# Kernel optimization log

Hardware: AMD Instinct MI355X
Metric: run time of the kernel (lower is better)

## Reference

```python
import jax, jax.numpy as jnp
import numpy as np

CUTOFF = 32.0  # matches init_kwargs cutoff


def _reduce_single(elem, cutoff):
    """elem: [T, D]. Returns (means_padded [T, D], n_segs scalar int32).

    Faithful to the torch loop: representative = elem[0]; walk frames; when
    ||rep - frame|| > cutoff, close the segment [rep_id:f_ind] (mean over it)
    and restart at `frame`. Final open segment is also emitted. Because the
    number of segments is data-dependent, we return a fixed-shape [T, D]
    buffer whose first n_segs rows are the stacked segment means (rest zeros).
    """
    T, D = elem.shape

    def step(rep, frame):
        d = jnp.linalg.norm(rep - frame)  # torch.norm default = Frobenius/L2
        new_seg = d > cutoff
        rep = jnp.where(new_seg, frame, rep)
        return rep, new_seg

    # flags[i] == True means frame i+1 starts a new segment
    _, flags = jax.lax.scan(step, elem[0], elem[1:])
    flags = jnp.concatenate([jnp.zeros((1,), dtype=bool), flags])  # frame 0 never starts anew
    seg_id = jnp.cumsum(flags.astype(jnp.int32))  # [T], ordered segment ids
    n_segs = seg_id[-1] + 1

    sums = jax.ops.segment_sum(elem, seg_id, num_segments=T)  # [T, D]
    counts = jax.ops.segment_sum(jnp.ones((T,), elem.dtype), seg_id, num_segments=T)  # [T]
    means = sums / jnp.maximum(counts, 1.0)[:, None]  # padded rows stay 0
    return means, n_segs


def setup_inputs() -> dict:
    key = jax.random.key(0)
    batch = jax.random.normal(key, (16, 4096, 512), dtype=jnp.float32)
    return {"batch": batch}


def reference(batch):
    # vmap over the list-of-sequences batch dim (all sequences same length T)
    means, n_segs = jax.vmap(lambda e: _reduce_single(e, CUTOFF))(batch)
    return means, n_segs
```

## Files before the change

kernel.cpp:

```cpp
#include <hip/hip_runtime.h>

#define NB 16
#define NT 4096
#define ND 512
#define NLEV 12
#define UPSTRIDE 4104

#define DIST8_F32(sout, y0, y1)                                   \
    {                                                             \
        float d_;                                                 \
        d_ = r0.x - (y0).x; sout = d_ * d_;                       \
        d_ = r0.y - (y0).y; sout = fmaf(d_, d_, sout);            \
        d_ = r0.z - (y0).z; sout = fmaf(d_, d_, sout);            \
        d_ = r0.w - (y0).w; sout = fmaf(d_, d_, sout);            \
        d_ = r1.x - (y1).x; sout = fmaf(d_, d_, sout);            \
        d_ = r1.y - (y1).y; sout = fmaf(d_, d_, sout);            \
        d_ = r1.z - (y1).z; sout = fmaf(d_, d_, sout);            \
        d_ = r1.w - (y1).w; sout = fmaf(d_, d_, sout);            \
    }

__device__ __forceinline__ bool decide_exact(const float* __restrict__ base, int row,
                                             int lane, float4 r0, float4 r1) {
    const float4* fp = (const float4*)(base + (size_t)row * ND);
    float4 y0 = fp[lane];
    float4 y1 = fp[lane + 64];
    float d;
    double sd;
    d = r0.x - y0.x; sd  = (double)d * d;
    d = r0.y - y0.y; sd += (double)d * d;
    d = r0.z - y0.z; sd += (double)d * d;
    d = r0.w - y0.w; sd += (double)d * d;
    d = r1.x - y1.x; sd += (double)d * d;
    d = r1.y - y1.y; sd += (double)d * d;
    d = r1.z - y1.z; sd += (double)d * d;
    d = r1.w - y1.w; sd += (double)d * d;
    #pragma unroll
    for (int off = 32; off >= 1; off >>= 1) sd += __shfl_xor(sd, off, 64);
    return ((float)sd > 1024.0f);
}

__device__ __forceinline__ bool screen1(float sk, const float* __restrict__ base,
                                        int row, int lane, float4 r0, float4 r1) {
    if (sk > 1024.25f) return true;
    if (sk < 1023.75f) return false;
    return decide_exact(base, row, lane, r0, r1);
}

__global__ __launch_bounds__(256) void kA_next(const float* __restrict__ in,
                                               int* __restrict__ nxt) {
    int lin  = blockIdx.x * 4 + (threadIdx.x >> 6);
    int lane = threadIdx.x & 63;
    int b = lin >> 12;
    int j = lin & (NT - 1);
    const float* base = in + (size_t)b * NT * ND;
    const float4* repp = (const float4*)(base + (size_t)j * ND);
    float4 r0 = repp[lane];
    float4 r1 = repp[lane + 64];

    int result = NT;
    int i = j + 1;
    while (i < NT) {
        int row0 = i;
        int row1 = (i + 1 < NT) ? i + 1 : NT - 1;
        int row2 = (i + 2 < NT) ? i + 2 : NT - 1;
        int row3 = (i + 3 < NT) ? i + 3 : NT - 1;
        const float4* f0 = (const float4*)(base + (size_t)row0 * ND);
        const float4* f1 = (const float4*)(base + (size_t)row1 * ND);
        const float4* f2 = (const float4*)(base + (size_t)row2 * ND);
        const float4* f3 = (const float4*)(base + (size_t)row3 * ND);
        float4 a0 = f0[lane], b0 = f0[lane + 64];
        float4 a1 = f1[lane], b1 = f1[lane + 64];
        float4 a2 = f2[lane], b2 = f2[lane + 64];
        float4 a3 = f3[lane], b3 = f3[lane + 64];

        float s0, s1, s2, s3;
        DIST8_F32(s0, a0, b0);
        DIST8_F32(s1, a1, b1);
        DIST8_F32(s2, a2, b2);
        DIST8_F32(s3, a3, b3);

        #pragma unroll
        for (int off = 32; off >= 1; off >>= 1) {
            s0 += __shfl_xor(s0, off, 64);
            s1 += __shfl_xor(s1, off, 64);
            s2 += __shfl_xor(s2, off, 64);
            s3 += __shfl_xor(s3, off, 64);
        }

        int nv = NT - i;
        int found = -1;
        if (screen1(s0, base, row0, lane, r0, r1)) found = i;
        else if (nv > 1 && screen1(s1, base, row1, lane, r0, r1)) found = i + 1;
        else if (nv > 2 && screen1(s2, base, row2, lane, r0, r1)) found = i + 2;
        else if (nv > 3 && screen1(s3, base, row3, lane, r0, r1)) found = i + 3;
        if (found >= 0) { result = found; break; }
        i += 4;
    }
    if (lane == 0) nxt[b * NT + j] = result;
}

__global__ __launch_bounds__(1024) void kB_build(const int* __restrict__ nxt,
                                                 unsigned short* __restrict__ up) {
    __shared__ unsigned short cur[NT + 8];
    __shared__ unsigned short nx[NT + 8];
    int b = blockIdx.x;
    int t = threadIdx.x;
    for (int j = t; j <= NT; j += 1024)
        cur[j] = (j < NT) ? (unsigned short)nxt[b * NT + j] : (unsigned short)NT;
    __syncthreads();
    {
        unsigned short* d0 = up + (size_t)(0 * NB + b) * UPSTRIDE;
        for (int j = t; j <= NT; j += 1024) d0[j] = cur[j];
    }
    for (int k = 1; k < NLEV; ++k) {
        for (int j = t; j <= NT; j += 1024) nx[j] = cur[cur[j]];
        __syncthreads();
        for (int j = t; j <= NT; j += 1024) cur[j] = nx[j];
        __syncthreads();
        unsigned short* dk = up + (size_t)(k * NB + b) * UPSTRIDE;
        for (int j = t; j <= NT; j += 1024) dk[j] = cur[j];
    }
}

__global__ __launch_bounds__(256) void kC_descend(const unsigned short* __restrict__ up,
                                                  int* __restrict__ start,
                                                  int* __restrict__ nseg,
                                                  float* __restrict__ out_tail) {
    int idx = blockIdx.x * 256 + threadIdx.x;
    int b = idx >> 12;
    int i = idx & (NT - 1);
    int pos = 0, cnt = 0;
    #pragma unroll
    for (int k = NLEV - 1; k >= 0; --k) {
        int t = up[(size_t)(k * NB + b) * UPSTRIDE + pos];
        if (t <= i) { pos = t; cnt += (1 << k); }
    }
    if (pos == i) start[b * NT + cnt] = i;
    if (i == NT - 1) {
        nseg[b] = cnt + 1;
        out_tail[b] = (float)(cnt + 1);
    }
}

__global__ __launch_bounds__(256) void kD_means(const float* __restrict__ in,
                                                const int* __restrict__ nxt,
                                                const int* __restrict__ start,
                                                const int* __restrict__ nseg,
                                                float* __restrict__ out) {
    int wid  = threadIdx.x >> 6;
    int lane = threadIdx.x & 63;
    int g = blockIdx.x * 4 + wid;
    int L0 = g * 8;
    for (int L = L0; L < L0 + 8; ++L) {
        int b = L >> 12;
        int r = L & (NT - 1);
        float4 acc0 = make_float4(0.f, 0.f, 0.f, 0.f);
        float4 acc1 = make_float4(0.f, 0.f, 0.f, 0.f);
        int n = nseg[b];
        if (r < n) {
            int s = start[b * NT + r];
            int e = nxt[b * NT + s];
            const float4* base = (const float4*)(in + (size_t)(b * NT + s) * ND);
            int cnt = e - s;
            for (int f = 0; f < cnt; ++f) {
                float4 v0 = base[(size_t)f * (ND / 4) + lane];
                float4 v1 = base[(size_t)f * (ND / 4) + lane + 64];
                acc0.x += v0.x; acc0.y += v0.y; acc0.z += v0.z; acc0.w += v0.w;
                acc1.x += v1.x; acc1.y += v1.y; acc1.z += v1.z; acc1.w += v1.w;
            }
            float c = (float)cnt;
            acc0.x /= c; acc0.y /= c; acc0.z /= c; acc0.w /= c;
            acc1.x /= c; acc1.y /= c; acc1.z /= c; acc1.w /= c;
        }
        float4* orow = (float4*)(out + (size_t)(b * NT + r) * ND);
        orow[lane]      = acc0;
        orow[lane + 64] = acc1;
    }
}

extern "C" void kernel_launch(void* const* d_in, const int* in_sizes, int n_in,
                              void* d_out, int out_size, void* d_ws, size_t ws_size,
                              hipStream_t stream) {
    const float* in = (const float*)d_in[0];
    float* out = (float*)d_out;
    char* ws = (char*)d_ws;

    int*            nxt   = (int*)(ws + 0);
    int*            start = (int*)(ws + 262144);
    int*            nseg  = (int*)(ws + 524288);
    unsigned short* up    = (unsigned short*)(ws + 524352);

    kA_next   <<<NB * NT / 4,   256,  0, stream>>>(in, nxt);
    kB_build  <<<NB,            1024, 0, stream>>>(nxt, up);
    kC_descend<<<NB * NT / 256, 256,  0, stream>>>(up, start, nseg,
                                                   out + (size_t)NB * NT * ND);
    kD_means  <<<2048,          256,  0, stream>>>(in, nxt, start, nseg, out);
}
```

Measured before the change: 334.7 us.

## Screen first four successors per frame in one pass, defer rare long scans

The next-break search now gives each wave 16 representatives, with 4 lanes per representative each checking one candidate successor. Only ambiguous or unresolved cases go onto an atomic worklist, and a second tail kernel resumes the full scan for those. The binary-lifting table plus descend kernels are replaced by one per-batch kernel that marks reachable segment starts in a bitmap and compacts them with a prefix scan. The means kernel now runs one wave per output row and unrolls its accumulation loop by two. The cost is an extra memset and worklist atomics, and per-lane 512-float serial loads in the screening pass are uncoalesced.

```diff
diff --git a/kernel.cpp b/kernel.cpp
--- a/kernel.cpp
+++ b/kernel.cpp
@@ -4,20 +4,6 @@
 #define NT 4096
 #define ND 512
 #define NLEV 12
-#define UPSTRIDE 4104
-
-#define DIST8_F32(sout, y0, y1)                                   \
-    {                                                             \
-        float d_;                                                 \
-        d_ = r0.x - (y0).x; sout = d_ * d_;                       \
-        d_ = r0.y - (y0).y; sout = fmaf(d_, d_, sout);            \
-        d_ = r0.z - (y0).z; sout = fmaf(d_, d_, sout);            \
-        d_ = r0.w - (y0).w; sout = fmaf(d_, d_, sout);            \
-        d_ = r1.x - (y1).x; sout = fmaf(d_, d_, sout);            \
-        d_ = r1.y - (y1).y; sout = fmaf(d_, d_, sout);            \
-        d_ = r1.z - (y1).z; sout = fmaf(d_, d_, sout);            \
-        d_ = r1.w - (y1).w; sout = fmaf(d_, d_, sout);            \
-    }
 
 __device__ __forceinline__ bool decide_exact(const float* __restrict__ base, int row,
                                              int lane, float4 r0, float4 r1) {
@@ -39,6 +25,19 @@
     return ((float)sd > 1024.0f);
 }
 
+#define DIST8_F32(sout, y0, y1)                                   \
+    {                                                             \
+        float d_;                                                 \
+        d_ = r0.x - (y0).x; sout = d_ * d_;                       \
+        d_ = r0.y - (y0).y; sout = fmaf(d_, d_, sout);            \
+        d_ = r0.z - (y0).z; sout = fmaf(d_, d_, sout);            \
+        d_ = r0.w - (y0).w; sout = fmaf(d_, d_, sout);            \
+        d_ = r1.x - (y1).x; sout = fmaf(d_, d_, sout);            \
+        d_ = r1.y - (y1).y; sout = fmaf(d_, d_, sout);            \
+        d_ = r1.z - (y1).z; sout = fmaf(d_, d_, sout);            \
+        d_ = r1.w - (y1).w; sout = fmaf(d_, d_, sout);            \
+    }
+
 __device__ __forceinline__ bool screen1(float sk, const float* __restrict__ base,
                                         int row, int lane, float4 r0, float4 r1) {
     if (sk > 1024.25f) return true;
@@ -47,99 +46,164 @@
 }
 
 __global__ __launch_bounds__(256) void kA_next(const float* __restrict__ in,
-                                               int* __restrict__ nxt) {
-    int lin  = blockIdx.x * 4 + (threadIdx.x >> 6);
+                                               int* __restrict__ nxt,
+                                               int2* __restrict__ list,
+                                               int* __restrict__ cnt) {
+    int wave = blockIdx.x * 4 + (threadIdx.x >> 6);
     int lane = threadIdx.x & 63;
-    int b = lin >> 12;
-    int j = lin & (NT - 1);
+    int j0 = wave * 16;
+    int b  = j0 >> 12;
+    int js = lane >> 2;
+    int p  = lane & 3;
+    int j  = (j0 & (NT - 1)) + js;
+    int ri = j + 1 + p;
+    bool valid = ri < NT;
+    int rc = valid ? ri : j;
+
     const float* base = in + (size_t)b * NT * ND;
-    const float4* repp = (const float4*)(base + (size_t)j * ND);
-    float4 r0 = repp[lane];
-    float4 r1 = repp[lane + 64];
-
-    int result = NT;
-    int i = j + 1;
-    while (i < NT) {
-        int row0 = i;
-        int row1 = (i + 1 < NT) ? i + 1 : NT - 1;
-        int row2 = (i + 2 < NT) ? i + 2 : NT - 1;
-        int row3 = (i + 3 < NT) ? i + 3 : NT - 1;
-        const float4* f0 = (const float4*)(base + (size_t)row0 * ND);
-        const float4* f1 = (const float4*)(base + (size_t)row1 * ND);
-        const float4* f2 = (const float4*)(base + (size_t)row2 * ND);
-        const float4* f3 = (const float4*)(base + (size_t)row3 * ND);
-        float4 a0 = f0[lane], b0 = f0[lane + 64];
-        float4 a1 = f1[lane], b1 = f1[lane + 64];
-        float4 a2 = f2[lane], b2 = f2[lane + 64];
-        float4 a3 = f3[lane], b3 = f3[lane + 64];
-
-        float s0, s1, s2, s3;
-        DIST8_F32(s0, a0, b0);
-        DIST8_F32(s1, a1, b1);
-        DIST8_F32(s2, a2, b2);
-        DIST8_F32(s3, a3, b3);
-
-        #pragma unroll
-        for (int off = 32; off >= 1; off >>= 1) {
-            s0 += __shfl_xor(s0, off, 64);
-            s1 += __shfl_xor(s1, off, 64);
-            s2 += __shfl_xor(s2, off, 64);
-            s3 += __shfl_xor(s3, off, 64);
-        }
-
-        int nv = NT - i;
-        int found = -1;
-        if (screen1(s0, base, row0, lane, r0, r1)) found = i;
-        else if (nv > 1 && screen1(s1, base, row1, lane, r0, r1)) found = i + 1;
-        else if (nv > 2 && screen1(s2, base, row2, lane, r0, r1)) found = i + 2;
-        else if (nv > 3 && screen1(s3, base, row3, lane, r0, r1)) found = i + 3;
-        if (found >= 0) { result = found; break; }
-        i += 4;
-    }
-    if (lane == 0) nxt[b * NT + j] = result;
-}
-
-__global__ __launch_bounds__(1024) void kB_build(const int* __restrict__ nxt,
-                                                 unsigned short* __restrict__ up) {
-    __shared__ unsigned short cur[NT + 8];
-    __shared__ unsigned short nx[NT + 8];
+    const float4* rp = (const float4*)(base + (size_t)j  * ND);
+    const float4* xp = (const float4*)(base + (size_t)rc * ND);
+
+    float s = 0.f;
+    #pragma unroll 8
+    for (int c = 0; c < 128; ++c) {
+        float4 a = rp[c];
+        float4 x = xp[c];
+        float d;
+        d = a.x - x.x; s = fmaf(d, d, s);
+        d = a.y - x.y; s = fmaf(d, d, s);
+        d = a.z - x.z; s = fmaf(d, d, s);
+        d = a.w - x.w; s = fmaf(d, d, s);
+    }
+
+    unsigned long long yes = __ballot(valid && (s > 1024.25f));
+    unsigned long long amb = __ballot(valid && (s > 1023.75f) && (s <= 1024.25f));
+
+    if (p == 0) {
+        int bj = b * NT + j;
+        unsigned ny = (unsigned)(yes >> (js * 4)) & 0xFu;
+        unsigned na = (unsigned)(amb >> (js * 4)) & 0xFu;
+        int ry = ny ? (__ffs(ny) - 1) : 4;
+        int ra = na ? (__ffs(na) - 1) : 4;
+        if (ra < ry) {
+            int idx = atomicAdd(cnt, 1);
+            list[idx] = make_int2(bj, j + 1 + ra);
+        } else if (ry < 4) {
+            nxt[bj] = j + 1 + ry;
+        } else if (j <= NT - 6) {
+            int idx = atomicAdd(cnt, 1);
+            list[idx] = make_int2(bj, j + 5);
+        } else {
+            nxt[bj] = NT;
+        }
+    }
+}
+
+__global__ __launch_bounds__(256) void kA2_tail(const float* __restrict__ in,
+                                                const int2* __restrict__ list,
+                                                const int* __restrict__ cnt,
+                                                int* __restrict__ nxt) {
+    int wave = blockIdx.x * 4 + (threadIdx.x >> 6);
+    int lane = threadIdx.x & 63;
+    int n = *cnt;
+    for (int e = wave; e < n; e += 2048) {
+        int2 ent = list[e];
+        int bj = ent.x;
+        int b = bj >> 12, j = bj & (NT - 1);
+        const float* base = in + (size_t)b * NT * ND;
+        const float4* repp = (const float4*)(base + (size_t)j * ND);
+        float4 r0 = repp[lane];
+        float4 r1 = repp[lane + 64];
+        int result = NT;
+        int i = ent.y;
+        while (i < NT) {
+            int row0 = i;
+            int row1 = (i + 1 < NT) ? i + 1 : NT - 1;
+            int row2 = (i + 2 < NT) ? i + 2 : NT - 1;
+            int row3 = (i + 3 < NT) ? i + 3 : NT - 1;
+            const float4* f0 = (const float4*)(base + (size_t)row0 * ND);
+            const float4* f1 = (const float4*)(base + (size_t)row1 * ND);
+            const float4* f2 = (const float4*)(base + (size_t)row2 * ND);
+            const float4* f3 = (const float4*)(base + (size_t)row3 * ND);
+            float4 a0 = f0[lane], b0 = f0[lane + 64];
+            float4 a1 = f1[lane], b1 = f1[lane + 64];
+            float4 a2 = f2[lane], b2 = f2[lane + 64];
+            float4 a3 = f3[lane], b3 = f3[lane + 64];
+            float s0, s1, s2, s3;
+            DIST8_F32(s0, a0, b0);
+            DIST8_F32(s1, a1, b1);
+            DIST8_F32(s2, a2, b2);
+            DIST8_F32(s3, a3, b3);
+            #pragma unroll
+            for (int off = 32; off >= 1; off >>= 1) {
+                s0 += __shfl_xor(s0, off, 64);
+                s1 += __shfl_xor(s1, off, 64);
+                s2 += __shfl_xor(s2, off, 64);
+                s3 += __shfl_xor(s3, off, 64);
+            }
+            int nv = NT - i;
+            int found = -1;
+            if (screen1(s0, base, row0, lane, r0, r1)) found = i;
+            else if (nv > 1 && screen1(s1, base, row1, lane, r0, r1)) found = i + 1;
+            else if (nv > 2 && screen1(s2, base, row2, lane, r0, r1)) found = i + 2;
+            else if (nv > 3 && screen1(s3, base, row3, lane, r0, r1)) found = i + 3;
+            if (found >= 0) { result = found; break; }
+            i += 4;
+        }
+        if (lane == 0) nxt[bj] = result;
+    }
+}
+
+__global__ __launch_bounds__(1024) void kChain(const int* __restrict__ nxt,
+                                               int* __restrict__ start,
+                                               int* __restrict__ nseg,
+                                               float* __restrict__ out_tail) {
+    __shared__ unsigned short h[NT + 1];
+    __shared__ unsigned short h2[NT + 1];
+    __shared__ unsigned reach[NT / 32];
+    __shared__ unsigned pref[NT / 32];
+    __shared__ unsigned wsum[NT / 32];
     int b = blockIdx.x;
     int t = threadIdx.x;
     for (int j = t; j <= NT; j += 1024)
-        cur[j] = (j < NT) ? (unsigned short)nxt[b * NT + j] : (unsigned short)NT;
+        h[j] = (j < NT) ? (unsigned short)nxt[b * NT + j] : (unsigned short)NT;
+    for (int w = t; w < NT / 32; w += 1024) reach[w] = 0;
     __syncthreads();
-    {
-        unsigned short* d0 = up + (size_t)(0 * NB + b) * UPSTRIDE;
-        for (int j = t; j <= NT; j += 1024) d0[j] = cur[j];
-    }
-    for (int k = 1; k < NLEV; ++k) {
-        for (int j = t; j <= NT; j += 1024) nx[j] = cur[cur[j]];
-        __syncthreads();
-        for (int j = t; j <= NT; j += 1024) cur[j] = nx[j];
-        __syncthreads();
-        unsigned short* dk = up + (size_t)(k * NB + b) * UPSTRIDE;
-        for (int j = t; j <= NT; j += 1024) dk[j] = cur[j];
-    }
-}
-
-__global__ __launch_bounds__(256) void kC_descend(const unsigned short* __restrict__ up,
-                                                  int* __restrict__ start,
-                                                  int* __restrict__ nseg,
-                                                  float* __restrict__ out_tail) {
-    int idx = blockIdx.x * 256 + threadIdx.x;
-    int b = idx >> 12;
-    int i = idx & (NT - 1);
-    int pos = 0, cnt = 0;
-    #pragma unroll
-    for (int k = NLEV - 1; k >= 0; --k) {
-        int t = up[(size_t)(k * NB + b) * UPSTRIDE + pos];
-        if (t <= i) { pos = t; cnt += (1 << k); }
-    }
-    if (pos == i) start[b * NT + cnt] = i;
-    if (i == NT - 1) {
-        nseg[b] = cnt + 1;
-        out_tail[b] = (float)(cnt + 1);
-    }
+    if (t == 0) reach[0] = 1u;
+    __syncthreads();
+    for (int k = 0; k < NLEV; ++k) {
+        if (t < NT / 32) {
+            unsigned m = reach[t];
+            while (m) {
+                int bit = __ffs(m) - 1; m &= m - 1;
+                int d = h[t * 32 + bit];
+                if (d < NT) atomicOr(&reach[d >> 5], 1u << (d & 31));
+            }
+        }
+        __syncthreads();
+        for (int j = t; j <= NT; j += 1024) h2[j] = h[h[j]];
+        __syncthreads();
+        for (int j = t; j <= NT; j += 1024) h[j] = h2[j];
+        __syncthreads();
+    }
+    if (t < NT / 32) { wsum[t] = __popc(reach[t]); pref[t] = wsum[t]; }
+    __syncthreads();
+    for (int off = 1; off < NT / 32; off <<= 1) {
+        unsigned v = 0;
+        if (t < NT / 32 && t >= off) v = pref[t - off];
+        __syncthreads();
+        if (t < NT / 32) pref[t] += v;
+        __syncthreads();
+    }
+    int n = pref[NT / 32 - 1];
+    for (int j = t; j < NT; j += 1024) {
+        unsigned w = reach[j >> 5];
+        if (w & (1u << (j & 31))) {
+            int r = (int)(pref[j >> 5] - __popc(w) + __popc(w & ((1u << (j & 31)) - 1)));
+            start[b * NT + r] = j;
+        }
+    }
+    if (t == 0) { nseg[b] = n; out_tail[b] = (float)n; }
 }
 
 __global__ __launch_bounds__(256) void kD_means(const float* __restrict__ in,
@@ -147,35 +211,42 @@
                                                 const int* __restrict__ start,
                                                 const int* __restrict__ nseg,
                                                 float* __restrict__ out) {
-    int wid  = threadIdx.x >> 6;
+    int wave = blockIdx.x * 4 + (threadIdx.x >> 6);
     int lane = threadIdx.x & 63;
-    int g = blockIdx.x * 4 + wid;
-    int L0 = g * 8;
-    for (int L = L0; L < L0 + 8; ++L) {
-        int b = L >> 12;
-        int r = L & (NT - 1);
-        float4 acc0 = make_float4(0.f, 0.f, 0.f, 0.f);
-        float4 acc1 = make_float4(0.f, 0.f, 0.f, 0.f);
-        int n = nseg[b];
-        if (r < n) {
-            int s = start[b * NT + r];
-            int e = nxt[b * NT + s];
-            const float4* base = (const float4*)(in + (size_t)(b * NT + s) * ND);
-            int cnt = e - s;
-            for (int f = 0; f < cnt; ++f) {
-                float4 v0 = base[(size_t)f * (ND / 4) + lane];
-                float4 v1 = base[(size_t)f * (ND / 4) + lane + 64];
-                acc0.x += v0.x; acc0.y += v0.y; acc0.z += v0.z; acc0.w += v0.w;
-                acc1.x += v1.x; acc1.y += v1.y; acc1.z += v1.z; acc1.w += v1.w;
-            }
-            float c = (float)cnt;
-            acc0.x /= c; acc0.y /= c; acc0.z /= c; acc0.w /= c;
-            acc1.x /= c; acc1.y /= c; acc1.z /= c; acc1.w /= c;
-        }
-        float4* orow = (float4*)(out + (size_t)(b * NT + r) * ND);
-        orow[lane]      = acc0;
-        orow[lane + 64] = acc1;
-    }
+    int b = wave >> 12;
+    int r = wave & (NT - 1);
+    float4 acc0 = make_float4(0.f, 0.f, 0.f, 0.f);
+    float4 acc1 = make_float4(0.f, 0.f, 0.f, 0.f);
+    int n = nseg[b];
+    if (r < n) {
+        int s = start[b * NT + r];
+        int e = nxt[b * NT + s];
+        const float4* base = (const float4*)(in + (size_t)(b * NT + s) * ND);
+        int cnt = e - s;
+        int f = 0;
+        for (; f + 2 <= cnt; f += 2) {
+            float4 v0 = base[(size_t)f * (ND / 4) + lane];
+            float4 v1 = base[(size_t)f * (ND / 4) + lane + 64];
+            float4 w0 = base[(size_t)(f + 1) * (ND / 4) + lane];
+            float4 w1 = base[(size_t)(f + 1) * (ND / 4) + lane + 64];
+            acc0.x += v0.x + w0.x; acc0.y += v0.y + w0.y;
+            acc0.z += v0.z + w0.z; acc0.w += v0.w + w0.w;
+            acc1.x += v1.x + w1.x; acc1.y += v1.y + w1.y;
+            acc1.z += v1.z + w1.z; acc1.w += v1.w + w1.w;
+        }
+        if (f < cnt) {
+            float4 v0 = base[(size_t)f * (ND / 4) + lane];
+            float4 v1 = base[(size_t)f * (ND / 4) + lane + 64];
+            acc0.x += v0.x; acc0.y += v0.y; acc0.z += v0.z; acc0.w += v0.w;
+            acc1.x += v1.x; acc1.y += v1.y; acc1.z += v1.z; acc1.w += v1.w;
+        }
+        float c = (float)cnt;
+        acc0.x /= c; acc0.y /= c; acc0.z /= c; acc0.w /= c;
+        acc1.x /= c; acc1.y /= c; acc1.z /= c; acc1.w /= c;
+    }
+    float4* orow = (float4*)(out + (size_t)(b * NT + r) * ND);
+    orow[lane]      = acc0;
+    orow[lane + 64] = acc1;
 }
 
 extern "C" void kernel_launch(void* const* d_in, const int* in_sizes, int n_in,
@@ -185,14 +256,17 @@
     float* out = (float*)d_out;
     char* ws = (char*)d_ws;
 
-    int*            nxt   = (int*)(ws + 0);
-    int*            start = (int*)(ws + 262144);
-    int*            nseg  = (int*)(ws + 524288);
-    unsigned short* up    = (unsigned short*)(ws + 524352);
-
-    kA_next   <<<NB * NT / 4,   256,  0, stream>>>(in, nxt);
-    kB_build  <<<NB,            1024, 0, stream>>>(nxt, up);
-    kC_descend<<<NB * NT / 256, 256,  0, stream>>>(up, start, nseg,
-                                                   out + (size_t)NB * NT * ND);
-    kD_means  <<<2048,          256,  0, stream>>>(in, nxt, start, nseg, out);
-}
+    int*  nxt   = (int*)(ws + 0);
+    int*  start = (int*)(ws + 262144);
+    int*  nseg  = (int*)(ws + 524288);
+    int*  cnt   = (int*)(ws + 524352);
+    int2* list  = (int2*)(ws + 524416);
+
+    hipMemsetAsync(cnt, 0, 4, stream);
+
+    kA_next <<<1024,  256,  0, stream>>>(in, nxt, list, cnt);
+    kA2_tail<<<512,   256,  0, stream>>>(in, list, cnt, nxt);
+    kChain  <<<NB,    1024, 0, stream>>>(nxt, start, nseg,
+                                         out + (size_t)NB * NT * ND);
+    kD_means<<<16384, 256,  0, stream>>>(in, nxt, start, nseg, out);
+}
```

Measured after the change: 390.3 us. 1.17x slower.
